# Kernel optimization log

Measured on AMD Instinct MI355X. Metric: run time of the kernel, lower is better.

The kernel has to match this reference:

```python
import jax, jax.numpy as jnp
import numpy as np

N, E = 50000, 800000
D_IN, D_H, D_OUT = 128, 128, 64


def setup_inputs() -> dict:
    key = jax.random.key(0)
    ks = jax.random.split(key, 12)
    x = jax.random.normal(ks[0], (N, D_IN), dtype=jnp.float32)
    edge_index = jax.random.randint(ks[1], (2, E), 0, N, dtype=jnp.int64)
    s = 0.05
    return {
        "x": x,
        "edge_index": edge_index,
        # SAGEConv layer 0: in -> hidden. lin_l (neighbor path, with bias), lin_r (root, no bias)
        "Wl0": jax.random.normal(ks[2], (D_H, D_IN), dtype=jnp.float32) * s,
        "bl0": jnp.zeros((D_H,), dtype=jnp.float32),
        "Wr0": jax.random.normal(ks[3], (D_H, D_IN), dtype=jnp.float32) * s,
        # layer 1: hidden -> hidden
        "Wl1": jax.random.normal(ks[4], (D_H, D_H), dtype=jnp.float32) * s,
        "bl1": jnp.zeros((D_H,), dtype=jnp.float32),
        "Wr1": jax.random.normal(ks[5], (D_H, D_H), dtype=jnp.float32) * s,
        # layer 2: hidden -> out
        "Wl2": jax.random.normal(ks[6], (D_OUT, D_H), dtype=jnp.float32) * s,
        "bl2": jnp.zeros((D_OUT,), dtype=jnp.float32),
        "Wr2": jax.random.normal(ks[7], (D_OUT, D_H), dtype=jnp.float32) * s,
    }


def reference(x, edge_index, Wl0, bl0, Wr0, Wl1, bl1, Wr1, Wl2, bl2, Wr2):
    n = x.shape[0]
    src, dst = edge_index[0], edge_index[1]
    # in-degree of each target node (mean aggregation denominator)
    deg = jax.ops.segment_sum(jnp.ones_like(dst, dtype=x.dtype), dst, num_segments=n)
    inv_deg = (1.0 / jnp.maximum(deg, 1.0))[:, None]  # [N,1]; zero-degree -> sum is 0 anyway

    def sage_conv(h, Wl, bl, Wr):
        # mean-aggregate neighbor features: gather h[src], scatter-add to dst
        agg = jax.ops.segment_sum(h[src], dst, num_segments=n) * inv_deg  # [N, d]
        return agg @ Wl.T + bl + h @ Wr.T

    h = jax.nn.relu(sage_conv(x, Wl0, bl0, Wr0))
    # dropout p=0 in eval mode (training=False, force_dropout=False) -> no-op
    h = jax.nn.relu(sage_conv(h, Wl1, bl1, Wr1))
    return sage_conv(h, Wl2, bl2, Wr2)
```

## Files before the change

kernel.cpp:

```cpp
#include <hip/hip_runtime.h>


#define D_H 128
#define NBUCKET 196
#define EPB 8192
#define NBLK 98

typedef _Float16 half8  __attribute__((ext_vector_type(8)));
typedef _Float16 half4v __attribute__((ext_vector_type(4)));
typedef float    floatx4 __attribute__((ext_vector_type(4)));

__global__ __launch_bounds__(256) void hist_wconv_kernel(
        const int* __restrict__ dst, int* __restrict__ histo, int E,
        const float* __restrict__ w0, const float* __restrict__ w1,
        const float* __restrict__ w2, const float* __restrict__ w3,
        const float* __restrict__ w4, const float* __restrict__ w5,
        _Float16* __restrict__ o0, _Float16* __restrict__ o1,
        _Float16* __restrict__ o2, _Float16* __restrict__ o3,
        _Float16* __restrict__ o4, _Float16* __restrict__ o5) {
    if (blockIdx.x < NBLK) {
        __shared__ int h[NBUCKET];
        for (int i = threadIdx.x; i < NBUCKET; i += 256) h[i] = 0;
        __syncthreads();
        int base = blockIdx.x * EPB;
        int end = min(base + EPB, E);
        for (int i = base + threadIdx.x; i < end; i += 256)
            atomicAdd(&h[dst[i] >> 8], 1);
        __syncthreads();
        for (int i = threadIdx.x; i < NBUCKET; i += 256)
            histo[blockIdx.x * NBUCKET + i] = h[i];
        return;
    }
    int k = (blockIdx.x - NBLK) * 256 + threadIdx.x;
    const float* in; _Float16* out; int j;
    if      (k <  4096) { in = w0; out = o0; j = k; }
    else if (k <  8192) { in = w1; out = o1; j = k - 4096; }
    else if (k < 12288) { in = w2; out = o2; j = k - 8192; }
    else if (k < 16384) { in = w3; out = o3; j = k - 12288; }
    else if (k < 18432) { in = w4; out = o4; j = k - 16384; }
    else if (k < 20480) { in = w5; out = o5; j = k - 18432; }
    else return;
    float4 v = ((const float4*)in)[j];
    half4v o = { (_Float16)v.x, (_Float16)v.y, (_Float16)v.z, (_Float16)v.w };
    ((half4v*)out)[j] = o;
}

__device__ __forceinline__ void dual_tile_f32(
        const float* __restrict__ Af,
        const _Float16* __restrict__ Wl, const _Float16* __restrict__ Wr,
        const float* __restrict__ bias,
        _Float16* __restrict__ T, _Float16* __restrict__ R,
        int N, int g) {
    const int ntile = (N + 63) >> 6;
    if (g >= 2 * ntile) return;
    const bool rpass = g >= ntile;
    const _Float16* __restrict__ W = rpass ? Wr : Wl;
    _Float16* __restrict__ O = rpass ? R : T;
    const int tile = rpass ? g - ntile : g;
    const int lt   = threadIdx.x & 127;
    const int wave = lt >> 6;
    const int lane = lt & 63;
    const int r16  = lane & 15;
    const int quad = lane >> 4;
    const int base = tile * 64 + wave * 32;
    const int koff = quad * 8;
    const int row0 = min(base + r16,      N - 1);
    const int row1 = min(base + 16 + r16, N - 1);

    floatx4 acc[2][8];
    #pragma unroll
    for (int s = 0; s < 2; ++s)
        #pragma unroll
        for (int j = 0; j < 8; ++j)
            acc[s][j] = (floatx4){0.f, 0.f, 0.f, 0.f};

    #pragma unroll
    for (int k0 = 0; k0 < 128; k0 += 32) {
        float4 p0 = *(const float4*)&Af[(size_t)row0 * 128 + k0 + koff];
        float4 p1 = *(const float4*)&Af[(size_t)row0 * 128 + k0 + koff + 4];
        float4 q0 = *(const float4*)&Af[(size_t)row1 * 128 + k0 + koff];
        float4 q1 = *(const float4*)&Af[(size_t)row1 * 128 + k0 + koff + 4];
        half8 a0 = (half8){ (_Float16)p0.x, (_Float16)p0.y, (_Float16)p0.z, (_Float16)p0.w,
                            (_Float16)p1.x, (_Float16)p1.y, (_Float16)p1.z, (_Float16)p1.w };
        half8 a1 = (half8){ (_Float16)q0.x, (_Float16)q0.y, (_Float16)q0.z, (_Float16)q0.w,
                            (_Float16)q1.x, (_Float16)q1.y, (_Float16)q1.z, (_Float16)q1.w };
        #pragma unroll
        for (int j = 0; j < 8; ++j) {
            half8 b = *(const half8*)&W[(size_t)(j * 16 + r16) * 128 + k0 + koff];
            acc[0][j] = __builtin_amdgcn_mfma_f32_16x16x32_f16(a0, b, acc[0][j], 0, 0, 0);
            acc[1][j] = __builtin_amdgcn_mfma_f32_16x16x32_f16(a1, b, acc[1][j], 0, 0, 0);
        }
    }

    #pragma unroll
    for (int s = 0; s < 2; ++s)
        #pragma unroll
        for (int i = 0; i < 4; ++i) {
            int r = base + s * 16 + quad * 4 + i;
            if (r >= N) continue;
            #pragma unroll
            for (int j = 0; j < 8; ++j) {
                int c = j * 16 + r16;
                float v = acc[s][j][i];
                if (rpass) v += bias[c];
                O[(size_t)r * 128 + c] = (_Float16)v;
            }
        }
}

__global__ __launch_bounds__(256) void scan_gemm_kernel(
        const int* __restrict__ histo, int* __restrict__ offs,
        int* __restrict__ boff, int* __restrict__ row_ptr, int n,
        const float* __restrict__ x, const _Float16* __restrict__ Wl,
        const _Float16* __restrict__ Wr, const float* __restrict__ bias,
        _Float16* __restrict__ T, _Float16* __restrict__ R, int gofs) {
    if (blockIdx.x == 0) {
        __shared__ int s[256];
        int t = threadIdx.x;
        int sum = 0;
        if (t < NBUCKET) {
            for (int b = 0; b < NBLK; ++b) {
                offs[b * NBUCKET + t] = sum;
                sum += histo[b * NBUCKET + t];
            }
        }
        s[t] = (t < NBUCKET) ? sum : 0;
        int tot = s[t];
        __syncthreads();
        for (int off = 1; off < 256; off <<= 1) {
            int tmp = (t >= off) ? s[t - off] : 0;
            __syncthreads();
            s[t] += tmp;
            __syncthreads();
        }
        int base = s[t] - tot;
        if (t < NBUCKET) boff[t] = base;
        if (t == 255) { boff[NBUCKET] = s[255]; row_ptr[n] = s[255]; }
        __syncthreads();
        if (t < NBUCKET)
            for (int b = 0; b < NBLK; ++b)
                offs[b * NBUCKET + t] += base;
        return;
    }
    int g = (blockIdx.x - 1) * 2 + (threadIdx.x >> 7) + gofs;
    dual_tile_f32(x, Wl, Wr, bias, T, R, n, g);
}

__global__ __launch_bounds__(256) void scatter_gemm_kernel(
        const int* __restrict__ src, const int* __restrict__ dst,
        const int* __restrict__ offs, unsigned int* __restrict__ bedge, int E,
        const float* __restrict__ x, const _Float16* __restrict__ Wl,
        const _Float16* __restrict__ Wr, const float* __restrict__ bias,
        _Float16* __restrict__ T, _Float16* __restrict__ R, int N, int gofs) {
    if (blockIdx.x < NBLK) {
        __shared__ int lcur[NBUCKET];
        for (int i = threadIdx.x; i < NBUCKET; i += 256)
            lcur[i] = offs[blockIdx.x * NBUCKET + i];
        __syncthreads();
        int base = blockIdx.x * EPB;
        int end = min(base + EPB, E);
        for (int i = base + threadIdx.x; i < end; i += 256) {
            int d = dst[i];
            int pos = atomicAdd(&lcur[d >> 8], 1);
            bedge[pos] = ((unsigned int)(d & 255) << 16) | (unsigned int)src[i];
        }
        return;
    }
    int g = (blockIdx.x - NBLK) * 2 + (threadIdx.x >> 7) + gofs;
    dual_tile_f32(x, Wl, Wr, bias, T, R, N, g);
}

__global__ __launch_bounds__(256) void bucket_gemm_kernel(
        const unsigned int* __restrict__ bedge, const int* __restrict__ boff,
        int* __restrict__ row_ptr, float* __restrict__ inv_deg,
        int* __restrict__ col, int n,
        const float* __restrict__ x, const _Float16* __restrict__ Wl,
        const _Float16* __restrict__ Wr, const float* __restrict__ bias,
        _Float16* __restrict__ T, _Float16* __restrict__ R, int gofs) {
    if (blockIdx.x < NBUCKET) {
        __shared__ int sdeg[256];
        __shared__ int sscan[256];
        __shared__ int lcur[256];
        const int b = blockIdx.x;
        const int t = threadIdx.x;
        const int base = boff[b];
        const int bend = boff[b + 1];
        sdeg[t] = 0;
        __syncthreads();
        for (int i = base + t; i < bend; i += 256)
            atomicAdd(&sdeg[bedge[i] >> 16], 1);
        __syncthreads();
        int d = sdeg[t];
        sscan[t] = d;
        __syncthreads();
        for (int off = 1; off < 256; off <<= 1) {
            int tmp = (t >= off) ? sscan[t - off] : 0;
            __syncthreads();
            sscan[t] += tmp;
            __syncthreads();
        }
        int excl = sscan[t] - d;
        int node = b * 256 + t;
        if (node < n) {
            row_ptr[node] = base + excl;
            inv_deg[node] = 1.0f / (float)max(d, 1);
        }
        lcur[t] = excl;
        __syncthreads();
        for (int i = base + t; i < bend; i += 256) {
            unsigned int v = bedge[i];
            int pos = atomicAdd(&lcur[v >> 16], 1);
            col[base + pos] = (int)(v & 0xffffu);
        }
        return;
    }
    int g = (blockIdx.x - NBUCKET) * 2 + (threadIdx.x >> 7) + gofs;
    dual_tile_f32(x, Wl, Wr, bias, T, R, n, g);
}

__global__ __launch_bounds__(128, 8) void agg_relu_kernel(
        const _Float16* __restrict__ T, const _Float16* __restrict__ R,
        const int* __restrict__ row_ptr, const int* __restrict__ col,
        const float* __restrict__ inv_deg, _Float16* __restrict__ h, int n) {
    int wave = threadIdx.x >> 6;
    int lane = threadIdx.x & 63;
    int node = blockIdx.x * 2 + wave;
    if (node >= n) return;
    int beg = row_ptr[node];
    int end = row_ptr[node + 1];
    const int quarter = lane >> 4;
    const int off = (lane & 15) << 3;
    float a0f = 0.f, a1f = 0.f, a2f = 0.f, a3f = 0.f;
    float a4f = 0.f, a5f = 0.f, a6f = 0.f, a7f = 0.f;
    for (int base = beg; base < end; base += 64) {
        int m = end - base;
        if (m > 64) m = 64;
        int myc = (lane < m) ? col[base + lane] : 0;
        int t = 0;
        for (; t + 4 <= (m >> 2); t += 4) {
            int u0 = __shfl(myc, ((t + 0) << 2) + quarter);
            int u1 = __shfl(myc, ((t + 1) << 2) + quarter);
            int u2 = __shfl(myc, ((t + 2) << 2) + quarter);
            int u3 = __shfl(myc, ((t + 3) << 2) + quarter);
            half8 v0 = *(const half8*)&T[(size_t)u0 * D_H + off];
            half8 v1 = *(const half8*)&T[(size_t)u1 * D_H + off];
            half8 v2 = *(const half8*)&T[(size_t)u2 * D_H + off];
            half8 v3 = *(const half8*)&T[(size_t)u3 * D_H + off];
            a0f += (float)v0[0] + (float)v1[0] + (float)v2[0] + (float)v3[0];
            a1f += (float)v0[1] + (float)v1[1] + (float)v2[1] + (float)v3[1];
            a2f += (float)v0[2] + (float)v1[2] + (float)v2[2] + (float)v3[2];
            a3f += (float)v0[3] + (float)v1[3] + (float)v2[3] + (float)v3[3];
            a4f += (float)v0[4] + (float)v1[4] + (float)v2[4] + (float)v3[4];
            a5f += (float)v0[5] + (float)v1[5] + (float)v2[5] + (float)v3[5];
            a6f += (float)v0[6] + (float)v1[6] + (float)v2[6] + (float)v3[6];
            a7f += (float)v0[7] + (float)v1[7] + (float)v2[7] + (float)v3[7];
        }
        int smax = (m + 3) >> 2;
        for (; t < smax; ++t) {
            int j = (t << 2) + quarter;
            int u = __shfl(myc, j);
            if (j < m) {
                half8 v = *(const half8*)&T[(size_t)u * D_H + off];
                a0f += (float)v[0]; a1f += (float)v[1];
                a2f += (float)v[2]; a3f += (float)v[3];
                a4f += (float)v[4]; a5f += (float)v[5];
                a6f += (float)v[6]; a7f += (float)v[7];
            }
        }
    }
    a0f += __shfl(a0f, lane + 16); a1f += __shfl(a1f, lane + 16);
    a2f += __shfl(a2f, lane + 16); a3f += __shfl(a3f, lane + 16);
    a4f += __shfl(a4f, lane + 16); a5f += __shfl(a5f, lane + 16);
    a6f += __shfl(a6f, lane + 16); a7f += __shfl(a7f, lane + 16);
    a0f += __shfl(a0f, lane + 32); a1f += __shfl(a1f, lane + 32);
    a2f += __shfl(a2f, lane + 32); a3f += __shfl(a3f, lane + 32);
    a4f += __shfl(a4f, lane + 32); a5f += __shfl(a5f, lane + 32);
    a6f += __shfl(a6f, lane + 32); a7f += __shfl(a7f, lane + 32);
    if (quarter == 0) {
        float s = inv_deg[node];
        half8 r = *(const half8*)&R[(size_t)node * D_H + off];
        half8 o = { (_Float16)fmaxf((float)r[0] + a0f * s, 0.f),
                    (_Float16)fmaxf((float)r[1] + a1f * s, 0.f),
                    (_Float16)fmaxf((float)r[2] + a2f * s, 0.f),
                    (_Float16)fmaxf((float)r[3] + a3f * s, 0.f),
                    (_Float16)fmaxf((float)r[4] + a4f * s, 0.f),
                    (_Float16)fmaxf((float)r[5] + a5f * s, 0.f),
                    (_Float16)fmaxf((float)r[6] + a6f * s, 0.f),
                    (_Float16)fmaxf((float)r[7] + a7f * s, 0.f) };
        *(half8*)&h[(size_t)node * D_H + off] = o;
    }
}

__global__ __launch_bounds__(128, 8) void aggregate_kernel(const _Float16* __restrict__ h,
                                                           const int* __restrict__ row_ptr,
                                                           const int* __restrict__ col,
                                                           const float* __restrict__ inv_deg,
                                                           _Float16* __restrict__ agg, int n) {
    int wave = threadIdx.x >> 6;
    int lane = threadIdx.x & 63;
    int node = blockIdx.x * 2 + wave;
    if (node >= n) return;
    int beg = row_ptr[node];
    int end = row_ptr[node + 1];
    const int quarter = lane >> 4;
    const int off = (lane & 15) << 3;
    float a0f = 0.f, a1f = 0.f, a2f = 0.f, a3f = 0.f;
    float a4f = 0.f, a5f = 0.f, a6f = 0.f, a7f = 0.f;
    for (int base = beg; base < end; base += 64) {
        int m = end - base;
        if (m > 64) m = 64;
        int myc = (lane < m) ? col[base + lane] : 0;
        int t = 0;
        for (; t + 4 <= (m >> 2); t += 4) {
            int u0 = __shfl(myc, ((t + 0) << 2) + quarter);
            int u1 = __shfl(myc, ((t + 1) << 2) + quarter);
            int u2 = __shfl(myc, ((t + 2) << 2) + quarter);
            int u3 = __shfl(myc, ((t + 3) << 2) + quarter);
            half8 v0 = *(const half8*)&h[(size_t)u0 * D_H + off];
            half8 v1 = *(const half8*)&h[(size_t)u1 * D_H + off];
            half8 v2 = *(const half8*)&h[(size_t)u2 * D_H + off];
            half8 v3 = *(const half8*)&h[(size_t)u3 * D_H + off];
            a0f += (float)v0[0] + (float)v1[0] + (float)v2[0] + (float)v3[0];
            a1f += (float)v0[1] + (float)v1[1] + (float)v2[1] + (float)v3[1];
            a2f += (float)v0[2] + (float)v1[2] + (float)v2[2] + (float)v3[2];
            a3f += (float)v0[3] + (float)v1[3] + (float)v2[3] + (float)v3[3];
            a4f += (float)v0[4] + (float)v1[4] + (float)v2[4] + (float)v3[4];
            a5f += (float)v0[5] + (float)v1[5] + (float)v2[5] + (float)v3[5];
            a6f += (float)v0[6] + (float)v1[6] + (float)v2[6] + (float)v3[6];
            a7f += (float)v0[7] + (float)v1[7] + (float)v2[7] + (float)v3[7];
        }
        int smax = (m + 3) >> 2;
        for (; t < smax; ++t) {
            int j = (t << 2) + quarter;
            int u = __shfl(myc, j);
            if (j < m) {
                half8 v = *(const half8*)&h[(size_t)u * D_H + off];
                a0f += (float)v[0]; a1f += (float)v[1];
                a2f += (float)v[2]; a3f += (float)v[3];
                a4f += (float)v[4]; a5f += (float)v[5];
                a6f += (float)v[6]; a7f += (float)v[7];
            }
        }
    }
    a0f += __shfl(a0f, lane + 16); a1f += __shfl(a1f, lane + 16);
    a2f += __shfl(a2f, lane + 16); a3f += __shfl(a3f, lane + 16);
    a4f += __shfl(a4f, lane + 16); a5f += __shfl(a5f, lane + 16);
    a6f += __shfl(a6f, lane + 16); a7f += __shfl(a7f, lane + 16);
    a0f += __shfl(a0f, lane + 32); a1f += __shfl(a1f, lane + 32);
    a2f += __shfl(a2f, lane + 32); a3f += __shfl(a3f, lane + 32);
    a4f += __shfl(a4f, lane + 32); a5f += __shfl(a5f, lane + 32);
    a6f += __shfl(a6f, lane + 32); a7f += __shfl(a7f, lane + 32);
    if (quarter == 0) {
        float s = inv_deg[node];
        half8 o = { (_Float16)(a0f * s), (_Float16)(a1f * s),
                    (_Float16)(a2f * s), (_Float16)(a3f * s),
                    (_Float16)(a4f * s), (_Float16)(a5f * s),
                    (_Float16)(a6f * s), (_Float16)(a7f * s) };
        *(half8*)&agg[(size_t)node * D_H + off] = o;
    }
}

template<int NT, bool RELU_HALF_OUT>
__global__ __launch_bounds__(128) void gemm_mfma_kernel(
        const _Float16* __restrict__ Xa, const _Float16* __restrict__ Xh,
        const _Float16* __restrict__ Wa, const _Float16* __restrict__ Wh,
        const float* __restrict__ bias,
        _Float16* __restrict__ out_h, float* __restrict__ out_f, int N) {
    const int wave = threadIdx.x >> 6;
    const int lane = threadIdx.x & 63;
    const int r16 = lane & 15;
    const int quad = lane >> 4;
    const int base = blockIdx.x * 64 + wave * 32;
    const int koff = quad * 8;

    floatx4 acc[2][NT];
    #pragma unroll
    for (int s = 0; s < 2; ++s)
        #pragma unroll
        for (int j = 0; j < NT; ++j)
            acc[s][j] = (floatx4){0.f, 0.f, 0.f, 0.f};

    #pragma unroll
    for (int hsel = 0; hsel < 2; ++hsel) {
        const _Float16* __restrict__ X = hsel ? Xh : Xa;
        const _Float16* __restrict__ W = hsel ? Wh : Wa;
        #pragma unroll
        for (int k0 = 0; k0 < 128; k0 += 32) {
            half8 a0 = *(const half8*)&X[(size_t)(base + r16) * 128 + k0 + koff];
            half8 a1 = *(const half8*)&X[(size_t)(base + 16 + r16) * 128 + k0 + koff];
            #pragma unroll
            for (int j = 0; j < NT; ++j) {
                half8 b = *(const half8*)&W[(size_t)(j * 16 + r16) * 128 + k0 + koff];
                acc[0][j] = __builtin_amdgcn_mfma_f32_16x16x32_f16(a0, b, acc[0][j], 0, 0, 0);
                acc[1][j] = __builtin_amdgcn_mfma_f32_16x16x32_f16(a1, b, acc[1][j], 0, 0, 0);
            }
        }
    }

    #pragma unroll
    for (int s = 0; s < 2; ++s) {
        #pragma unroll
        for (int i = 0; i < 4; ++i) {
            int r = base + s * 16 + quad * 4 + i;
            if (r >= N) continue;
            #pragma unroll
            for (int j = 0; j < NT; ++j) {
                int c = j * 16 + r16;
                float v = acc[s][j][i] + bias[c];
                if (RELU_HALF_OUT) {
                    v = fmaxf(v, 0.f);
                    out_h[(size_t)r * (NT * 16) + c] = (_Float16)v;
                } else {
                    out_f[(size_t)r * (NT * 16) + c] = v;
                }
            }
        }
    }
}

__global__ __launch_bounds__(128) void gemm_dual_kernel(
        const _Float16* __restrict__ B, const _Float16* __restrict__ Wl,
        const _Float16* __restrict__ Wr, const float* __restrict__ bias,
        _Float16* __restrict__ T, _Float16* __restrict__ Rh, int N) {
    const int wave = threadIdx.x >> 6;
    const int lane = threadIdx.x & 63;
    const int r16 = lane & 15;
    const int quad = lane >> 4;
    const int base = blockIdx.x * 64 + wave * 32;
    const int koff = quad * 8;

    floatx4 accT[2][4], accR[2][4];
    #pragma unroll
    for (int s = 0; s < 2; ++s)
        #pragma unroll
        for (int j = 0; j < 4; ++j) {
            accT[s][j] = (floatx4){0.f, 0.f, 0.f, 0.f};
            accR[s][j] = (floatx4){0.f, 0.f, 0.f, 0.f};
        }

    #pragma unroll
    for (int k0 = 0; k0 < 128; k0 += 32) {
        half8 a0 = *(const half8*)&B[(size_t)(base + r16) * 128 + k0 + koff];
        half8 a1 = *(const half8*)&B[(size_t)(base + 16 + r16) * 128 + k0 + koff];
        #pragma unroll
        for (int j = 0; j < 4; ++j) {
            half8 bl = *(const half8*)&Wl[(size_t)(j * 16 + r16) * 128 + k0 + koff];
            half8 br = *(const half8*)&Wr[(size_t)(j * 16 + r16) * 128 + k0 + koff];
            accT[0][j] = __builtin_amdgcn_mfma_f32_16x16x32_f16(a0, bl, accT[0][j], 0, 0, 0);
            accT[1][j] = __builtin_amdgcn_mfma_f32_16x16x32_f16(a1, bl, accT[1][j], 0, 0, 0);
            accR[0][j] = __builtin_amdgcn_mfma_f32_16x16x32_f16(a0, br, accR[0][j], 0, 0, 0);
            accR[1][j] = __builtin_amdgcn_mfma_f32_16x16x32_f16(a1, br, accR[1][j], 0, 0, 0);
        }
    }

    #pragma unroll
    for (int s = 0; s < 2; ++s) {
        #pragma unroll
        for (int i = 0; i < 4; ++i) {
            int r = base + s * 16 + quad * 4 + i;
            if (r >= N) continue;
            #pragma unroll
            for (int j = 0; j < 4; ++j) {
                int c = j * 16 + r16;
                T[(size_t)r * 64 + c]  = (_Float16)accT[s][j][i];
                Rh[(size_t)r * 64 + c] = (_Float16)(accR[s][j][i] + bias[c]);
            }
        }
    }
}

__global__ __launch_bounds__(128, 8) void aggregate_add64_kernel(
        const _Float16* __restrict__ T,
        const _Float16* __restrict__ Rh,
        const int* __restrict__ row_ptr,
        const int* __restrict__ col,
        const float* __restrict__ inv_deg,
        float* __restrict__ out, int n) {
    int wave = threadIdx.x >> 6;
    int lane = threadIdx.x & 63;
    int node = blockIdx.x * 2 + wave;
    if (node >= n) return;
    int beg = row_ptr[node];
    int end = row_ptr[node + 1];
    const int quarter = lane >> 4;
    const int off = (lane & 15) << 2;
    float a0f = 0.f, a1f = 0.f, a2f = 0.f, a3f = 0.f;
    for (int base = beg; base < end; base += 64) {
        int m = end - base;
        if (m > 64) m = 64;
        int myc = (lane < m) ? col[base + lane] : 0;
        int t = 0;
        for (; t + 4 <= (m >> 2); t += 4) {
            int u0 = __shfl(myc, ((t + 0) << 2) + quarter);
            int u1 = __shfl(myc, ((t + 1) << 2) + quarter);
            int u2 = __shfl(myc, ((t + 2) << 2) + quarter);
            int u3 = __shfl(myc, ((t + 3) << 2) + quarter);
            half4v v0 = *(const half4v*)&T[(size_t)u0 * 64 + off];
            half4v v1 = *(const half4v*)&T[(size_t)u1 * 64 + off];
            half4v v2 = *(const half4v*)&T[(size_t)u2 * 64 + off];
            half4v v3 = *(const half4v*)&T[(size_t)u3 * 64 + off];
            a0f += (float)v0[0] + (float)v1[0] + (float)v2[0] + (float)v3[0];
            a1f += (float)v0[1] + (float)v1[1] + (float)v2[1] + (float)v3[1];
            a2f += (float)v0[2] + (float)v1[2] + (float)v2[2] + (float)v3[2];
            a3f += (float)v0[3] + (float)v1[3] + (float)v2[3] + (float)v3[3];
        }
        int smax = (m + 3) >> 2;
        for (; t < smax; ++t) {
            int j = (t << 2) + quarter;
            int u = __shfl(myc, j);
            if (j < m) {
                half4v v = *(const half4v*)&T[(size_t)u * 64 + off];
                a0f += (float)v[0]; a1f += (float)v[1];
                a2f += (float)v[2]; a3f += (float)v[3];
            }
        }
    }
    a0f += __shfl(a0f, lane + 16); a1f += __shfl(a1f, lane + 16);
    a2f += __shfl(a2f, lane + 16); a3f += __shfl(a3f, lane + 16);
    a0f += __shfl(a0f, lane + 32); a1f += __shfl(a1f, lane + 32);
    a2f += __shfl(a2f, lane + 32); a3f += __shfl(a3f, lane + 32);
    if (quarter == 0) {
        float s = inv_deg[node];
        half4v r = *(const half4v*)&Rh[(size_t)node * 64 + off];
        float4 o;
        o.x = (float)r[0] + a0f * s;
        o.y = (float)r[1] + a1f * s;
        o.z = (float)r[2] + a2f * s;
        o.w = (float)r[3] + a3f * s;
        *(float4*)&out[(size_t)node * 64 + off] = o;
    }
}

extern "C" void kernel_launch(void* const* d_in, const int* in_sizes, int n_in,
                              void* d_out, int out_size, void* d_ws, size_t ws_size,
                              hipStream_t stream) {
    const float* x   = (const float*)d_in[0];
    const int*   edge = (const int*)d_in[1];
    const float* Wl0 = (const float*)d_in[2];
    const float* bl0 = (const float*)d_in[3];
    const float* Wr0 = (const float*)d_in[4];
    const float* Wl1 = (const float*)d_in[5];
    const float* bl1 = (const float*)d_in[6];
    const float* Wr1 = (const float*)d_in[7];
    const float* Wl2 = (const float*)d_in[8];
    const float* bl2 = (const float*)d_in[9];
    const float* Wr2 = (const float*)d_in[10];
    float* out = (float*)d_out;

    const int N = in_sizes[0] / D_H;
    const int E = in_sizes[1] / 2;
    const int* src = edge;
    const int* dst = edge + E;

    const int gx = (N + 63) / 64;
    const int Np = gx * 64;
    const size_t HBYTES = (size_t)Np * D_H * 2;

    char* w = (char*)d_ws;
    _Float16* Tb = (_Float16*)w;  w += HBYTES;
    _Float16* Rb = (_Float16*)w;  w += HBYTES;
    _Float16* Hb = (_Float16*)w;  w += HBYTES;
    _Float16* Wl0h = (_Float16*)w;  w += (size_t)128 * 128 * 2;
    _Float16* Wr0h = (_Float16*)w;  w += (size_t)128 * 128 * 2;
    _Float16* Wl1h = (_Float16*)w;  w += (size_t)128 * 128 * 2;
    _Float16* Wr1h = (_Float16*)w;  w += (size_t)128 * 128 * 2;
    _Float16* Wl2h = (_Float16*)w;  w += (size_t)64 * 128 * 2;
    _Float16* Wr2h = (_Float16*)w;  w += (size_t)64 * 128 * 2;
    int* row_ptr = (int*)w;      w += (size_t)(N + 16) * 4;
    float* inv_deg = (float*)w;  w += (size_t)N * 4;
    int* col     = (int*)w;      w += (size_t)E * 4;
    int* histo   = (int*)w;      w += (size_t)NBLK * NBUCKET * 4;
    int* offs    = (int*)w;      w += (size_t)NBLK * NBUCKET * 4;
    int* boff    = (int*)w;      w += (size_t)(NBUCKET + 1) * 4;
    unsigned int* bedge = (unsigned int*)w;  w += (size_t)E * 4;

    _Float16* T2  = (_Float16*)Hb;
    _Float16* Rh2 = (_Float16*)((char*)Hb + HBYTES / 2);

    hist_wconv_kernel<<<NBLK + 80, 256, 0, stream>>>(
        dst, histo, E,
        Wl0, Wr0, Wl1, Wr1, Wl2, Wr2,
        Wl0h, Wr0h, Wl1h, Wr1h, Wl2h, Wr2h);

    const int C0 = 260, C1 = 260, C2 = gx - C0 - C1;
    scan_gemm_kernel<<<1 + C0, 256, 0, stream>>>(
        histo, offs, boff, row_ptr, N,
        x, Wl0h, Wr0h, bl0, Tb, Rb, 0);
    scatter_gemm_kernel<<<NBLK + C1, 256, 0, stream>>>(
        src, dst, offs, bedge, E,
        x, Wl0h, Wr0h, bl0, Tb, Rb, N, 2 * C0);
    bucket_gemm_kernel<<<NBUCKET + C2, 256, 0, stream>>>(
        bedge, boff, row_ptr, inv_deg, col, N,
        x, Wl0h, Wr0h, bl0, Tb, Rb, 2 * (C0 + C1));

    const int agg_grid = (N + 1) / 2;

    agg_relu_kernel<<<agg_grid, 128, 0, stream>>>(Tb, Rb, row_ptr, col, inv_deg, Hb, N);

    aggregate_kernel<<<agg_grid, 128, 0, stream>>>(Hb, row_ptr, col, inv_deg, Rb, N);
    gemm_mfma_kernel<8, true><<<gx, 128, 0, stream>>>(Rb, Hb, Wl1h, Wr1h, bl1, Tb, nullptr, N);

    gemm_dual_kernel<<<gx, 128, 0, stream>>>(Tb, Wl2h, Wr2h, bl2, T2, Rh2, N);
    aggregate_add64_kernel<<<agg_grid, 128, 0, stream>>>(T2, Rh2, row_ptr, col,
                                                         inv_deg, out, N);
}
```

Before: 288.6 us.

## Fuse layer-1 GEMM with layer-2 dual GEMM via shared-memory hidden tile

Merges the layer-1 MFMA GEMM (bias+ReLU, half output) and the layer-2 dual-projection GEMM into one kernel. Each block keeps its 64-row ReLU'd hidden tile in LDS and feeds it straight into the second GEMM, so the N×128 half hidden tensor is never written to or reread from global memory and one launch is removed. The T2/Rh2 outputs now alias Tb instead of Hb. The cost is extra LDS per block (about 17KB) plus a block barrier, which may reduce occupancy.

```diff
diff --git a/kernel.cpp b/kernel.cpp
--- a/kernel.cpp
+++ b/kernel.cpp
@@ -360,12 +360,14 @@
     }
 }
 
-template<int NT, bool RELU_HALF_OUT>
-__global__ __launch_bounds__(128) void gemm_mfma_kernel(
+__global__ __launch_bounds__(128) void fused_l1l2_kernel(
         const _Float16* __restrict__ Xa, const _Float16* __restrict__ Xh,
         const _Float16* __restrict__ Wa, const _Float16* __restrict__ Wh,
-        const float* __restrict__ bias,
-        _Float16* __restrict__ out_h, float* __restrict__ out_f, int N) {
+        const float* __restrict__ b1,
+        const _Float16* __restrict__ Wl2, const _Float16* __restrict__ Wr2,
+        const float* __restrict__ b2,
+        _Float16* __restrict__ T2, _Float16* __restrict__ Rh2, int N) {
+    __shared__ _Float16 hs[64][136];
     const int wave = threadIdx.x >> 6;
     const int lane = threadIdx.x & 63;
     const int r16 = lane & 15;
@@ -373,61 +375,44 @@
     const int base = blockIdx.x * 64 + wave * 32;
     const int koff = quad * 8;
 
-    floatx4 acc[2][NT];
-    #pragma unroll
-    for (int s = 0; s < 2; ++s)
-        #pragma unroll
-        for (int j = 0; j < NT; ++j)
-            acc[s][j] = (floatx4){0.f, 0.f, 0.f, 0.f};
-
-    #pragma unroll
-    for (int hsel = 0; hsel < 2; ++hsel) {
-        const _Float16* __restrict__ X = hsel ? Xh : Xa;
-        const _Float16* __restrict__ W = hsel ? Wh : Wa;
-        #pragma unroll
-        for (int k0 = 0; k0 < 128; k0 += 32) {
-            half8 a0 = *(const half8*)&X[(size_t)(base + r16) * 128 + k0 + koff];
-            half8 a1 = *(const half8*)&X[(size_t)(base + 16 + r16) * 128 + k0 + koff];
+    {
+        floatx4 acc[2][8];
+        #pragma unroll
+        for (int s = 0; s < 2; ++s)
             #pragma unroll
-            for (int j = 0; j < NT; ++j) {
-                half8 b = *(const half8*)&W[(size_t)(j * 16 + r16) * 128 + k0 + koff];
-                acc[0][j] = __builtin_amdgcn_mfma_f32_16x16x32_f16(a0, b, acc[0][j], 0, 0, 0);
-                acc[1][j] = __builtin_amdgcn_mfma_f32_16x16x32_f16(a1, b, acc[1][j], 0, 0, 0);
-            }
-        }
-    }
-
-    #pragma unroll
-    for (int s = 0; s < 2; ++s) {
-        #pragma unroll
-        for (int i = 0; i < 4; ++i) {
-            int r = base + s * 16 + quad * 4 + i;
-            if (r >= N) continue;
+            for (int j = 0; j < 8; ++j)
+                acc[s][j] = (floatx4){0.f, 0.f, 0.f, 0.f};
+
+        #pragma unroll
+        for (int hsel = 0; hsel < 2; ++hsel) {
+            const _Float16* __restrict__ X = hsel ? Xh : Xa;
+            const _Float16* __restrict__ W = hsel ? Wh : Wa;
             #pragma unroll
-            for (int j = 0; j < NT; ++j) {
-                int c = j * 16 + r16;
-                float v = acc[s][j][i] + bias[c];
-                if (RELU_HALF_OUT) {
-                    v = fmaxf(v, 0.f);
-                    out_h[(size_t)r * (NT * 16) + c] = (_Float16)v;
-                } else {
-                    out_f[(size_t)r * (NT * 16) + c] = v;
+            for (int k0 = 0; k0 < 128; k0 += 32) {
+                half8 a0 = *(const half8*)&X[(size_t)(base + r16) * 128 + k0 + koff];
+                half8 a1 = *(const half8*)&X[(size_t)(base + 16 + r16) * 128 + k0 + koff];
+                #pragma unroll
+                for (int j = 0; j < 8; ++j) {
+                    half8 b = *(const half8*)&W[(size_t)(j * 16 + r16) * 128 + k0 + koff];
+                    acc[0][j] = __builtin_amdgcn_mfma_f32_16x16x32_f16(a0, b, acc[0][j], 0, 0, 0);
+                    acc[1][j] = __builtin_amdgcn_mfma_f32_16x16x32_f16(a1, b, acc[1][j], 0, 0, 0);
                 }
             }
         }
-    }
-}
-
-__global__ __launch_bounds__(128) void gemm_dual_kernel(
-        const _Float16* __restrict__ B, const _Float16* __restrict__ Wl,
-        const _Float16* __restrict__ Wr, const float* __restrict__ bias,
-        _Float16* __restrict__ T, _Float16* __restrict__ Rh, int N) {
-    const int wave = threadIdx.x >> 6;
-    const int lane = threadIdx.x & 63;
-    const int r16 = lane & 15;
-    const int quad = lane >> 4;
-    const int base = blockIdx.x * 64 + wave * 32;
-    const int koff = quad * 8;
+
+        #pragma unroll
+        for (int s = 0; s < 2; ++s)
+            #pragma unroll
+            for (int i = 0; i < 4; ++i) {
+                int lr = wave * 32 + s * 16 + quad * 4 + i;
+                #pragma unroll
+                for (int j = 0; j < 8; ++j) {
+                    int c = j * 16 + r16;
+                    hs[lr][c] = (_Float16)fmaxf(acc[s][j][i] + b1[c], 0.f);
+                }
+            }
+    }
+    __syncthreads();
 
     floatx4 accT[2][4], accR[2][4];
     #pragma unroll
@@ -440,12 +425,12 @@
 
     #pragma unroll
     for (int k0 = 0; k0 < 128; k0 += 32) {
-        half8 a0 = *(const half8*)&B[(size_t)(base + r16) * 128 + k0 + koff];
-        half8 a1 = *(const half8*)&B[(size_t)(base + 16 + r16) * 128 + k0 + koff];
+        half8 a0 = *(const half8*)&hs[wave * 32 + r16][k0 + koff];
+        half8 a1 = *(const half8*)&hs[wave * 32 + 16 + r16][k0 + koff];
         #pragma unroll
         for (int j = 0; j < 4; ++j) {
-            half8 bl = *(const half8*)&Wl[(size_t)(j * 16 + r16) * 128 + k0 + koff];
-            half8 br = *(const half8*)&Wr[(size_t)(j * 16 + r16) * 128 + k0 + koff];
+            half8 bl = *(const half8*)&Wl2[(size_t)(j * 16 + r16) * 128 + k0 + koff];
+            half8 br = *(const half8*)&Wr2[(size_t)(j * 16 + r16) * 128 + k0 + koff];
             accT[0][j] = __builtin_amdgcn_mfma_f32_16x16x32_f16(a0, bl, accT[0][j], 0, 0, 0);
             accT[1][j] = __builtin_amdgcn_mfma_f32_16x16x32_f16(a1, bl, accT[1][j], 0, 0, 0);
             accR[0][j] = __builtin_amdgcn_mfma_f32_16x16x32_f16(a0, br, accR[0][j], 0, 0, 0);
@@ -462,8 +447,8 @@
             #pragma unroll
             for (int j = 0; j < 4; ++j) {
                 int c = j * 16 + r16;
-                T[(size_t)r * 64 + c]  = (_Float16)accT[s][j][i];
-                Rh[(size_t)r * 64 + c] = (_Float16)(accR[s][j][i] + bias[c]);
+                T2[(size_t)r * 64 + c]  = (_Float16)accT[s][j][i];
+                Rh2[(size_t)r * 64 + c] = (_Float16)(accR[s][j][i] + b2[c]);
             }
         }
     }
@@ -574,8 +559,8 @@
     int* boff    = (int*)w;      w += (size_t)(NBUCKET + 1) * 4;
     unsigned int* bedge = (unsigned int*)w;  w += (size_t)E * 4;
 
-    _Float16* T2  = (_Float16*)Hb;
-    _Float16* Rh2 = (_Float16*)((char*)Hb + HBYTES / 2);
+    _Float16* T2  = (_Float16*)Tb;
+    _Float16* Rh2 = (_Float16*)((char*)Tb + HBYTES / 2);
 
     hist_wconv_kernel<<<NBLK + 80, 256, 0, stream>>>(
         dst, histo, E,
@@ -598,9 +583,10 @@
     agg_relu_kernel<<<agg_grid, 128, 0, stream>>>(Tb, Rb, row_ptr, col, inv_deg, Hb, N);
 
     aggregate_kernel<<<agg_grid, 128, 0, stream>>>(Hb, row_ptr, col, inv_deg, Rb, N);
-    gemm_mfma_kernel<8, true><<<gx, 128, 0, stream>>>(Rb, Hb, Wl1h, Wr1h, bl1, Tb, nullptr, N);
-
-    gemm_dual_kernel<<<gx, 128, 0, stream>>>(Tb, Wl2h, Wr2h, bl2, T2, Rh2, N);
+
+    fused_l1l2_kernel<<<gx, 128, 0, stream>>>(Rb, Hb, Wl1h, Wr1h, bl1,
+                                              Wl2h, Wr2h, bl2, T2, Rh2, N);
+
     aggregate_add64_kernel<<<agg_grid, 128, 0, stream>>>(T2, Rh2, row_ptr, col,
                                                          inv_deg, out, N);
 }
```

Result: faster. 279.6 us, median of 2 (-3.1%).
